# Kernel optimization log

Measured on AMD Instinct MI355X. Metric: run time of the kernel, lower is better.

## Reference

```python
import jax, jax.numpy as jnp
import numpy as np

S, B, D, H, DFF = 1024, 8, 1024, 16, 4096
HD = D // H
EPS = 1e-5


def layernorm(x, g, b):
    m = jnp.mean(x, axis=-1, keepdims=True)
    v = jnp.mean(jnp.square(x - m), axis=-1, keepdims=True)
    return (x - m) * jax.lax.rsqrt(v + EPS) * g + b


def setup_inputs() -> dict:
    key = jax.random.key(0)
    ks = jax.random.split(key, 6)
    w = 0.02
    return {
        "src": jax.random.normal(ks[0], (S, B, D), dtype=jnp.float32),
        "in_proj_w": jax.random.normal(ks[1], (3 * D, D), dtype=jnp.float32) * w,
        "in_proj_b": jnp.zeros((3 * D,), dtype=jnp.float32),
        "out_w": jax.random.normal(ks[2], (D, D), dtype=jnp.float32) * w,
        "out_b": jnp.zeros((D,), dtype=jnp.float32),
        "lin1_w": jax.random.normal(ks[3], (DFF, D), dtype=jnp.float32) * w,
        "lin1_b": jnp.zeros((DFF,), dtype=jnp.float32),
        "lin2_w": jax.random.normal(ks[4], (D, DFF), dtype=jnp.float32) * w,
        "lin2_b": jnp.zeros((D,), dtype=jnp.float32),
        "n1_g": jnp.ones((D,), dtype=jnp.float32),
        "n1_b": jnp.zeros((D,), dtype=jnp.float32),
        "n2_g": jnp.ones((D,), dtype=jnp.float32),
        "n2_b": jnp.zeros((D,), dtype=jnp.float32),
    }


def reference(src, in_proj_w, in_proj_b, out_w, out_b,
              lin1_w, lin1_b, lin2_w, lin2_b,
              n1_g, n1_b, n2_g, n2_b):
    # self-attention block (eval mode: dropout = identity)
    qkv = jnp.einsum('sbd,ed->sbe', src, in_proj_w) + in_proj_b  # [S,B,3D]
    q, k, v = jnp.split(qkv, 3, axis=-1)
    q = q.reshape(S, B, H, HD) * (1.0 / np.sqrt(HD)).astype(np.float32)
    k = k.reshape(S, B, H, HD)
    v = v.reshape(S, B, H, HD)
    scores = jnp.einsum('sbhd,tbhd->bhst', q, k)        # [B,H,S,S]
    attn = jax.nn.softmax(scores, axis=-1)
    o = jnp.einsum('bhst,tbhd->sbhd', attn, v).reshape(S, B, D)
    o = jnp.einsum('sbd,ed->sbe', o, out_w) + out_b
    # post-LN residuals
    x = layernorm(src + o, n1_g, n1_b)
    h = jax.nn.relu(jnp.einsum('sbd,fd->sbf', x, lin1_w) + lin1_b)
    f = jnp.einsum('sbf,df->sbd', h, lin2_w) + lin2_b
    return layernorm(x + f, n2_g, n2_b)
```

## Files before the change

### kernel.cpp

```cpp
#include <hip/hip_runtime.h>
#include <cstdint>
#include <cstddef>

#define S_  1024
#define B_  8
#define D_  1024
#define H_  16
#define HD_ 64
#define DFF_ 4096
#define M_  (S_*B_)
#define QKV_N (3*D_)

typedef float f32x4 __attribute__((ext_vector_type(4)));
typedef __bf16 bf16x8 __attribute__((ext_vector_type(8)));
typedef __bf16 bf16x4 __attribute__((ext_vector_type(4)));

#define GLDS16(gp, lp) __builtin_amdgcn_global_load_lds( \
    (__attribute__((address_space(1))) void*)(gp), \
    (__attribute__((address_space(3))) void*)(lp), 16, 0, 0)

#define CB0 (M_*D_/4)
#define CB1 (CB0 + QKV_N*D_/4)
#define CB2 (CB1 + D_*D_/4)
#define CB3 (CB2 + DFF_*D_/4)
#define CB4 (CB3 + D_*DFF_/4)

__global__ __launch_bounds__(256)
void cvt_all(const float* __restrict__ src, const float* __restrict__ w1f,
             const float* __restrict__ w2f, const float* __restrict__ w3f,
             const float* __restrict__ w4f,
             __bf16* __restrict__ src_bf, __bf16* __restrict__ w1,
             __bf16* __restrict__ w2, __bf16* __restrict__ w3,
             __bf16* __restrict__ w4)
{
    int i = blockIdx.x * 256 + threadIdx.x;
    const float* in; __bf16* out; int off;
    if      (i < CB0) { in = src; out = src_bf; off = 0;   }
    else if (i < CB1) { in = w1f; out = w1;     off = CB0; }
    else if (i < CB2) { in = w2f; out = w2;     off = CB1; }
    else if (i < CB3) { in = w3f; out = w3;     off = CB2; }
    else if (i < CB4) { in = w4f; out = w4;     off = CB3; }
    else return;
    int j = i - off;
    float4 v = *(const float4*)(in + (size_t)j * 4);
    __bf16 t[4] = {(__bf16)v.x, (__bf16)v.y, (__bf16)v.z, (__bf16)v.w};
    *(uint2*)(out + (size_t)j * 4) = *(uint2*)t;
}

template<bool OUT_BF16, bool RELU, bool ADD_BIAS, bool SPLITZ>
__global__ __launch_bounds__(512, 2)
void gemm8p(const __bf16* __restrict__ A, const __bf16* __restrict__ W,
            const float* __restrict__ bias,
            void* __restrict__ Cv0, void* __restrict__ Cv1,
            int N, int Kloop, int lda)
{
    extern __shared__ __bf16 lds[];

    const int tid  = threadIdx.x;
    const int lane = tid & 63;
    const int wv   = tid >> 6;
    const int quad = lane >> 4;
    const int l15  = lane & 15;
    const int wm   = (wv >> 2) * 128;
    const int wn   = (wv & 3) * 64;

    const int id  = blockIdx.y * gridDim.x + blockIdx.x;
    const int nwg = gridDim.x * gridDim.y;
    const int q8  = nwg >> 3;
    const int k   = (id & 7) * q8 + (id >> 3);
    const int within = k & 31;
    const int chunk  = k >> 5;
    const int nchm   = gridDim.x >> 3;
    const int cm     = chunk % nchm;
    const int cn     = chunk / nchm;
    const int m0 = (cm * 8 + (within & 7)) * 256;
    const int n0 = (cn * 4 + (within >> 3)) * 256;

    void* Cv = Cv0;
    if (SPLITZ) {
        const int koff = blockIdx.z * Kloop;
        A += koff;
        W += koff;
        if (blockIdx.z) Cv = Cv1;
    }

    const int nt = Kloop >> 6;

    const int crow = tid >> 2;
    const int csl  = (tid & 3) ^ ((crow >> 1) & 3);
    const __bf16* gA[2] = { A + (size_t)(m0 + crow) * lda + csl * 8,
                            A + (size_t)(m0 + 128 + crow) * lda + csl * 8 };
    const __bf16* gW[2] = { W + (size_t)(n0 + crow) * lda + csl * 8,
                            W + (size_t)(n0 + 128 + crow) * lda + csl * 8 };
    char* ldsSt = (char*)lds + tid * 16;

    #define CHA(kv, hh, kt) GLDS16(gA[hh] + ((kt) << 6) + (kv) * 32, \
        ldsSt + (((kt) & 1) * 65536 + (kv) * 16384 + (hh) * 8192))
    #define CHB(kv, hh, kt) GLDS16(gW[hh] + ((kt) << 6) + (kv) * 32, \
        ldsSt + (((kt) & 1) * 65536 + 32768 + (kv) * 16384 + (hh) * 8192))

    const int swzE = (quad ^ ((l15 >> 1) & 3)) * 8;
    const __bf16* aBase = lds + (wm + l15) * 32 + swzE;
    const __bf16* bBase = lds + 16384 + (wn + l15) * 32 + swzE;

    CHB(0,0,0); CHB(0,1,0); CHA(0,0,0); CHA(0,1,0);
    CHB(1,0,0); CHB(1,1,0); CHA(1,0,0); CHA(1,1,0);
    CHB(0,0,1); CHB(0,1,1); CHA(0,0,1); CHA(0,1,1);
    CHB(1,0,1); CHB(1,1,1);
    asm volatile("s_waitcnt vmcnt(6)" ::: "memory");
    __builtin_amdgcn_s_barrier();

    f32x4 acc[8][4] = {};

    #define KTILE(T, S1, S2, VM1, VM2) do { \
        const __bf16* aB = aBase + ((T) & 1) * 32768; \
        const __bf16* bB = bBase + ((T) & 1) * 32768; \
        bf16x8 b_[4], a_[4]; \
         \
        _Pragma("unroll") for (int j = 0; j < 4; ++j) b_[j] = *(const bf16x8*)(bB + j * 512); \
        _Pragma("unroll") for (int i = 0; i < 4; ++i) a_[i] = *(const bf16x8*)(aB + i * 512); \
        if (S1) { CHA(1,0,(T)+1); CHA(1,1,(T)+1); } \
        __builtin_amdgcn_s_barrier(); \
        asm volatile("s_waitcnt lgkmcnt(0)" ::: "memory"); \
        __builtin_amdgcn_s_setprio(1); \
        _Pragma("unroll") for (int i = 0; i < 4; ++i) \
            _Pragma("unroll") for (int j = 0; j < 4; ++j) \
                acc[i][j] = __builtin_amdgcn_mfma_f32_16x16x32_bf16(a_[i], b_[j], acc[i][j], 0, 0, 0); \
        __builtin_amdgcn_s_setprio(0); \
        __builtin_amdgcn_s_barrier(); \
         \
        _Pragma("unroll") for (int i = 0; i < 4; ++i) a_[i] = *(const bf16x8*)(aB + (i + 4) * 512); \
        if (S2) { CHB(0,0,(T)+2); CHB(0,1,(T)+2); } \
        __builtin_amdgcn_s_barrier(); \
        asm volatile("s_waitcnt lgkmcnt(0)" ::: "memory"); \
        __builtin_amdgcn_s_setprio(1); \
        _Pragma("unroll") for (int i = 0; i < 4; ++i) \
            _Pragma("unroll") for (int j = 0; j < 4; ++j) \
                acc[i+4][j] = __builtin_amdgcn_mfma_f32_16x16x32_bf16(a_[i], b_[j], acc[i+4][j], 0, 0, 0); \
        __builtin_amdgcn_s_setprio(0); \
        asm volatile("s_waitcnt vmcnt(" VM1 ")" ::: "memory"); \
        __builtin_amdgcn_s_barrier(); \
         \
        _Pragma("unroll") for (int j = 0; j < 4; ++j) b_[j] = *(const bf16x8*)(bB + 8192 + j * 512); \
        _Pragma("unroll") for (int i = 0; i < 4; ++i) a_[i] = *(const bf16x8*)(aB + 8192 + i * 512); \
        if (S2) { CHA(0,0,(T)+2); CHA(0,1,(T)+2); } \
        __builtin_amdgcn_s_barrier(); \
        asm volatile("s_waitcnt lgkmcnt(0)" ::: "memory"); \
        __builtin_amdgcn_s_setprio(1); \
        _Pragma("unroll") for (int i = 0; i < 4; ++i) \
            _Pragma("unroll") for (int j = 0; j < 4; ++j) \
                acc[i][j] = __builtin_amdgcn_mfma_f32_16x16x32_bf16(a_[i], b_[j], acc[i][j], 0, 0, 0); \
        __builtin_amdgcn_s_setprio(0); \
        __builtin_amdgcn_s_barrier(); \
         \
        _Pragma("unroll") for (int i = 0; i < 4; ++i) a_[i] = *(const bf16x8*)(aB + 8192 + (i + 4) * 512); \
        if (S2) { CHB(1,0,(T)+2); CHB(1,1,(T)+2); } \
        __builtin_amdgcn_s_barrier(); \
        asm volatile("s_waitcnt lgkmcnt(0)" ::: "memory"); \
        __builtin_amdgcn_s_setprio(1); \
        _Pragma("unroll") for (int i = 0; i < 4; ++i) \
            _Pragma("unroll") for (int j = 0; j < 4; ++j) \
                acc[i+4][j] = __builtin_amdgcn_mfma_f32_16x16x32_bf16(a_[i], b_[j], acc[i+4][j], 0, 0, 0); \
        __builtin_amdgcn_s_setprio(0); \
        asm volatile("s_waitcnt vmcnt(" VM2 ")" ::: "memory"); \
        __builtin_amdgcn_s_barrier(); \
    } while (0)

    for (int t = 0; t < nt - 2; ++t) KTILE(t, true, true, "10", "10");
    KTILE(nt - 2, true,  false, "8", "4");
    KTILE(nt - 1, false, false, "0", "0");

    #undef KTILE
    #undef CHA
    #undef CHB

    float bvj[4];
    #pragma unroll
    for (int j = 0; j < 4; ++j)
        bvj[j] = ADD_BIAS ? bias[n0 + wn + j * 16 + l15] : 0.f;
    const size_t cbase = (size_t)(m0 + wm + quad * 4) * N + (n0 + wn + l15);
    #pragma unroll
    for (int i = 0; i < 8; ++i) {
        #pragma unroll
        for (int r = 0; r < 4; ++r) {
            const size_t rowb = cbase + (size_t)(i * 16 + r) * N;
            #pragma unroll
            for (int j = 0; j < 4; ++j) {
                float v = acc[i][j][r] + bvj[j];
                if (RELU) v = fmaxf(v, 0.f);
                if (OUT_BF16)
                    ((__bf16*)Cv)[rowb + j * 16] = (__bf16)v;
                else
                    ((float*)Cv)[rowb + j * 16] = v;
            }
        }
    }
}

template<bool OUT_BF16, bool RELU, bool ADD_BIAS, bool SPLITZ>
__global__ __launch_bounds__(512, 4)
void gemm128(const __bf16* __restrict__ A, const __bf16* __restrict__ W,
             const float* __restrict__ bias,
             void* __restrict__ Cv0, void* __restrict__ Cv1,
             int N, int Kloop, int lda)
{
    extern __shared__ __bf16 lds[];

    const int tid  = threadIdx.x;
    const int lane = tid & 63;
    const int wv   = tid >> 6;
    const int quad = lane >> 4;
    const int l15  = lane & 15;
    const int wm   = (wv & 1) * 64;
    const int wn   = (wv >> 1) * 64;

    const int id  = blockIdx.y * gridDim.x + blockIdx.x;
    const int nwg = gridDim.x * gridDim.y;
    const int q8  = nwg >> 3;
    const int k   = (id & 7) * q8 + (id >> 3);
    const int within = k & 31;
    const int chunk  = k >> 5;
    const int nchm   = gridDim.x >> 3;
    const int cm     = chunk % nchm;
    const int cn     = chunk / nchm;
    const int m0 = (cm * 8 + (within & 7)) * 128;
    const int n0 = (cn * 4 + (within >> 3)) * 256;

    void* Cv = Cv0;
    if (SPLITZ) {
        const int koff = blockIdx.z * Kloop;
        A += koff;
        W += koff;
        if (blockIdx.z) Cv = Cv1;
    }

    const int nt = Kloop >> 5;

    const int crow = tid >> 2;
    const int csl  = (tid & 3) ^ ((crow >> 1) & 3);
    const __bf16* gA0 = A + (size_t)(m0 + crow) * lda + csl * 8;
    const __bf16* gW0 = W + (size_t)(n0 + crow) * lda + csl * 8;
    const __bf16* gW1 = gW0 + (size_t)128 * lda;
    char* ldsSt = (char*)lds + tid * 16;

    #define STAGE(kt, buf) do { \
        const int ko = (kt) << 5; \
        char* d_ = ldsSt + (buf) * 24576; \
        GLDS16(gW0 + ko, d_ + 8192); \
        GLDS16(gW1 + ko, d_ + 16384); \
        GLDS16(gA0 + ko, d_); \
    } while (0)

    const int swz = (quad ^ ((l15 >> 1) & 3)) * 8;
    const __bf16* aBase = lds + (wm + l15) * 32 + swz;
    const __bf16* bBase = lds + 4096 + (wn + l15) * 32 + swz;

    #define BARRIER_DRAIN() do { \
        asm volatile("s_waitcnt vmcnt(0)" ::: "memory"); \
        __builtin_amdgcn_s_barrier(); \
        __builtin_amdgcn_sched_barrier(0); \
    } while (0)

    STAGE(0, 0);
    BARRIER_DRAIN();

    f32x4 acc[4][4] = {};

    for (int t = 0; t < nt; ++t) {
        const int cur = t & 1;
        if (t + 1 < nt) STAGE(t + 1, cur ^ 1);

        const __bf16* aB = aBase + cur * 12288;
        const __bf16* bB = bBase + cur * 12288;
        bf16x8 b_[4];
        #pragma unroll
        for (int j = 0; j < 4; ++j)
            b_[j] = *(const bf16x8*)(bB + j * 512);
        __builtin_amdgcn_s_setprio(1);
        #pragma unroll
        for (int i = 0; i < 4; ++i) {
            bf16x8 a_ = *(const bf16x8*)(aB + i * 512);
            #pragma unroll
            for (int j = 0; j < 4; ++j)
                acc[i][j] = __builtin_amdgcn_mfma_f32_16x16x32_bf16(a_, b_[j], acc[i][j], 0, 0, 0);
        }
        __builtin_amdgcn_s_setprio(0);

        if (t + 1 < nt) BARRIER_DRAIN();
    }

    #undef BARRIER_DRAIN
    #undef STAGE

    float bvj[4];
    #pragma unroll
    for (int j = 0; j < 4; ++j)
        bvj[j] = ADD_BIAS ? bias[n0 + wn + j * 16 + l15] : 0.f;
    const size_t cbase = (size_t)(m0 + wm + quad * 4) * N + (n0 + wn + l15);
    #pragma unroll
    for (int i = 0; i < 4; ++i) {
        #pragma unroll
        for (int r = 0; r < 4; ++r) {
            const size_t rowb = cbase + (size_t)(i * 16 + r) * N;
            #pragma unroll
            for (int j = 0; j < 4; ++j) {
                float v = acc[i][j][r] + bvj[j];
                if (RELU) v = fmaxf(v, 0.f);
                if (OUT_BF16)
                    ((__bf16*)Cv)[rowb + j * 16] = (__bf16)v;
                else
                    ((float*)Cv)[rowb + j * 16] = v;
            }
        }
    }
}

__global__ __launch_bounds__(256)
void v_transpose(const __bf16* __restrict__ qkv, __bf16* __restrict__ vt)
{
    __shared__ __bf16 T[64 * 65];
    const int tid = threadIdx.x;
    const int t0  = blockIdx.x * 64;
    const int bh  = blockIdx.y;
    const int b   = bh & (B_ - 1);
    const int h   = bh / B_;

    #pragma unroll
    for (int j = 0; j < 2; ++j) {
        int c = j * 256 + tid;
        int i = c >> 3, cc = c & 7;
        const __bf16* g = qkv + (size_t)((t0 + i) * B_ + b) * QKV_N + 2 * D_ + h * HD_ + cc * 8;
        bf16x8 v = *(const bf16x8*)g;
        #pragma unroll
        for (int u = 0; u < 8; ++u) T[(cc * 8 + u) * 65 + i] = v[u];
    }
    __syncthreads();
    #pragma unroll
    for (int j = 0; j < 2; ++j) {
        int c = j * 256 + tid;
        int d = c >> 3, cc = c & 7;
        __bf16 pk[8];
        #pragma unroll
        for (int u = 0; u < 8; ++u) pk[u] = T[d * 65 + cc * 8 + u];
        *(uint4*)(vt + ((size_t)bh * HD_ + d) * S_ + t0 + cc * 8) = *(uint4*)pk;
    }
}

__global__ __launch_bounds__(512, 4)
void attn_flash(const __bf16* __restrict__ qkv, const __bf16* __restrict__ vt,
                __bf16* __restrict__ out)
{
    extern __shared__ __bf16 alds[];
    __bf16* Ks0 = alds;
    __bf16* Vs0 = alds + 16384;
    __bf16* Ps  = alds + 32768;

    const int tid  = threadIdx.x;
    const int lane = tid & 63;
    const int wv   = tid >> 6;
    const int quad = lane >> 4;
    const int l15  = lane & 15;

    const int id = blockIdx.y * gridDim.x + blockIdx.x;
    const int k  = (id & 7) * ((S_ / 128) * B_ * H_ / 8) + (id >> 3);
    const int s0 = (k & 7) * 128;
    const int bh = k >> 3;
    const int b  = bh & (B_ - 1);
    const int h  = bh / B_;

    const int i0k = tid >> 3, cck = tid & 7, scck = cck ^ (i0k & 7);
    const int i0v = tid >> 4, ccv = tid & 15, sccv = ccv ^ (i0v & 15);
    const __bf16* gK0 = qkv + ((size_t)i0k * B_ + b) * QKV_N + D_ + h * HD_ + scck * 8;
    const __bf16* gK1 = gK0 + (size_t)64 * B_ * QKV_N;
    const __bf16* gV0 = vt + ((size_t)bh * HD_ + i0v) * S_ + sccv * 8;
    const __bf16* gV1 = gV0 + (size_t)32 * S_;
    char* dK = (char*)Ks0 + tid * 16;
    char* dV = (char*)Vs0 + tid * 16;
    const size_t KADV = (size_t)128 * B_ * QKV_N;

    #define STAGEKV(buf) do { \
        GLDS16(gK0, dK + (buf) * 16384); \
        GLDS16(gK1, dK + (buf) * 16384 + 8192); \
        GLDS16(gV0, dV + (buf) * 16384); \
        GLDS16(gV1, dV + (buf) * 16384 + 8192); \
        gK0 += KADV; gK1 += KADV; gV0 += 128; gV1 += 128; \
    } while (0)

    STAGEKV(0);

    const int qrow = wv * 16 + l15;
    bf16x8 bq[2];
    #pragma unroll
    for (int kk = 0; kk < 2; ++kk)
        bq[kk] = *(const bf16x8*)(qkv + (size_t)((s0 + qrow) * B_ + b) * QKV_N
                                  + h * HD_ + kk * 32 + quad * 8);

    __syncthreads();

    f32x4 oacc[4] = {};
    float l_run = 0.f;
    const float C2 = 0.125f * 1.44269504f;
    const int xk = l15 & 7;
    const __bf16* psB = Ps + qrow * 64;

    const int nt2 = S_ / 128;
    for (int it = 0; it < nt2; ++it) {
        const int cur = it & 1;
        if (it + 1 < nt2) STAGEKV(cur ^ 1);

        #pragma unroll
        for (int s = 0; s < 2; ++s) {
            f32x4 sacc[4] = {};
            #pragma unroll
            for (int kk = 0; kk < 2; ++kk) {
                const __bf16* akB = Ks0 + cur * 8192 + s * 4096 + l15 * 64
                                    + (((kk * 4 + quad) ^ xk) * 8);
                #pragma unroll
                for (int j = 0; j < 4; ++j)
                    sacc[j] = __builtin_amdgcn_mfma_f32_16x16x32_bf16(
                        *(const bf16x8*)(akB + j * 1024), bq[kk], sacc[j], 0, 0, 0);
            }

            float rs = 0.f;
            #pragma unroll
            for (int j = 0; j < 4; ++j)
                #pragma unroll
                for (int r = 0; r < 4; ++r) {
                    float p = __builtin_amdgcn_exp2f(sacc[j][r] * C2);
                    sacc[j][r] = p;
                    rs += p;
                }
            rs += __shfl_xor(rs, 16, 64);
            rs += __shfl_xor(rs, 32, 64);
            l_run += rs;

            #pragma unroll
            for (int j = 0; j < 4; ++j) {
                __bf16 pk[4] = {(__bf16)sacc[j][0], (__bf16)sacc[j][1],
                                (__bf16)sacc[j][2], (__bf16)sacc[j][3]};
                int s16 = (j * 2 + (quad >> 1)) ^ xk;
                *(uint2*)(psB + s16 * 8 + (quad & 1) * 4) = *(uint2*)pk;
            }

            #pragma unroll
            for (int kk = 0; kk < 2; ++kk) {
                bf16x8 ap = *(const bf16x8*)(psB + (((kk * 4 + quad) ^ xk) * 8));
                const __bf16* bvB = Vs0 + cur * 8192 + l15 * 128
                                    + (((s * 8 + kk * 4 + quad) ^ l15) * 8);
                #pragma unroll
                for (int jd = 0; jd < 4; ++jd)
                    oacc[jd] = __builtin_amdgcn_mfma_f32_16x16x32_bf16(
                        ap, *(const bf16x8*)(bvB + jd * 2048), oacc[jd], 0, 0, 0);
            }
        }

        __syncthreads();
    }
    #undef STAGEKV

    float linv = 1.f / l_run;
    #pragma unroll
    for (int r = 0; r < 4; ++r) {
        float lr = __shfl(linv, quad * 4 + r, 64);
        int s = s0 + wv * 16 + quad * 4 + r;
        #pragma unroll
        for (int jd = 0; jd < 4; ++jd) {
            int d = jd * 16 + l15;
            out[(size_t)(s * B_ + b) * D_ + h * HD_ + d] = (__bf16)(oacc[jd][r] * lr);
        }
    }
}

__global__ __launch_bounds__(256)
void ln_res3(const float* __restrict__ xa, const __bf16* __restrict__ p0,
             const __bf16* __restrict__ p1, const float* __restrict__ bias,
             const float* __restrict__ g, const float* __restrict__ beta,
             float* __restrict__ yout, __bf16* __restrict__ ybf)
{
    __shared__ float red[8];
    const int row = blockIdx.x;
    const int tid = threadIdx.x;
    const size_t base = (size_t)row * D_ + tid * 4;

    float4 a  = *(const float4*)(xa + base);
    bf16x4 q0 = *(const bf16x4*)(p0 + base);
    bf16x4 q1 = *(const bf16x4*)(p1 + base);
    float4 bb = *(const float4*)(bias + tid * 4);
    float x0 = a.x + (float)q0[0] + (float)q1[0] + bb.x;
    float x1 = a.y + (float)q0[1] + (float)q1[1] + bb.y;
    float x2 = a.z + (float)q0[2] + (float)q1[2] + bb.z;
    float x3 = a.w + (float)q0[3] + (float)q1[3] + bb.w;

    float s  = x0 + x1 + x2 + x3;
    float ss = x0 * x0 + x1 * x1 + x2 * x2 + x3 * x3;
    for (int msk = 1; msk <= 32; msk <<= 1) {
        s  += __shfl_xor(s,  msk, 64);
        ss += __shfl_xor(ss, msk, 64);
    }
    const int wv = tid >> 6;
    if ((tid & 63) == 0) { red[wv] = s; red[4 + wv] = ss; }
    __syncthreads();
    s  = red[0] + red[1] + red[2] + red[3];
    ss = red[4] + red[5] + red[6] + red[7];
    float mean = s * (1.f / D_);
    float var  = ss * (1.f / D_) - mean * mean;
    float rstd = rsqrtf(var + 1e-5f);

    float4 gv = *(const float4*)(g + tid * 4);
    float4 bv = *(const float4*)(beta + tid * 4);
    float y0 = (x0 - mean) * rstd * gv.x + bv.x;
    float y1 = (x1 - mean) * rstd * gv.y + bv.y;
    float y2 = (x2 - mean) * rstd * gv.z + bv.z;
    float y3 = (x3 - mean) * rstd * gv.w + bv.w;
    *(float4*)(yout + base) = make_float4(y0, y1, y2, y3);
    if (ybf) {
        __bf16 t[4] = {(__bf16)y0, (__bf16)y1, (__bf16)y2, (__bf16)y3};
        *(uint2*)(ybf + base) = *(uint2*)t;
    }
}

extern "C" void kernel_launch(void* const* d_in, const int* in_sizes, int n_in,
                              void* d_out, int out_size, void* d_ws, size_t ws_size,
                              hipStream_t stream)
{
    const float* src       = (const float*)d_in[0];
    const float* in_proj_w = (const float*)d_in[1];
    const float* in_proj_b = (const float*)d_in[2];
    const float* out_w     = (const float*)d_in[3];
    const float* out_b     = (const float*)d_in[4];
    const float* lin1_w    = (const float*)d_in[5];
    const float* lin1_b    = (const float*)d_in[6];
    const float* lin2_w    = (const float*)d_in[7];
    const float* lin2_b    = (const float*)d_in[8];
    const float* n1_g = (const float*)d_in[9];
    const float* n1_b = (const float*)d_in[10];
    const float* n2_g = (const float*)d_in[11];
    const float* n2_b = (const float*)d_in[12];

    char* ws = (char*)d_ws;
    size_t off = 0;
    auto alloc = [&](size_t bytes) { char* p = ws + off; off += (bytes + 255) & ~(size_t)255; return p; };

    __bf16* src_bf = (__bf16*)alloc((size_t)M_ * D_ * 2);
    __bf16* w1     = (__bf16*)alloc((size_t)QKV_N * D_ * 2);
    __bf16* w2     = (__bf16*)alloc((size_t)D_ * D_ * 2);
    __bf16* w3     = (__bf16*)alloc((size_t)DFF_ * D_ * 2);
    __bf16* w4     = (__bf16*)alloc((size_t)D_ * DFF_ * 2);
    __bf16* qkv    = (__bf16*)alloc((size_t)M_ * QKV_N * 2);
    char*   h_r    = alloc((size_t)M_ * DFF_ * 2);
    __bf16* xbf    = (__bf16*)alloc((size_t)M_ * D_ * 2);
    float*  xf     = (float*)alloc((size_t)M_ * D_ * 4);
    __bf16* vt     = (__bf16*)alloc((size_t)B_ * H_ * HD_ * S_ * 2);

    const size_t PART = (size_t)M_ * D_;
    __bf16* attn_o = src_bf;
    __bf16* o0 = (__bf16*)h_r;
    __bf16* o1 = o0 + PART;
    __bf16* hbf = (__bf16*)h_r;
    __bf16* f0 = vt;
    __bf16* f1 = xbf;

    const size_t SHM8  = 131072;
    const size_t SHM2  = 49152;
    const size_t ASHM  = 81920;

    cvt_all<<<(CB4 + 255) / 256, 256, 0, stream>>>(
        src, in_proj_w, out_w, lin1_w, lin2_w, src_bf, w1, w2, w3, w4);

    gemm128<true, false, true, false><<<dim3(M_ / 128, QKV_N / 256), 512, SHM2, stream>>>(
        src_bf, w1, in_proj_b, qkv, nullptr, QKV_N, D_, D_);

    v_transpose<<<dim3(S_ / 64, B_ * H_), 256, 0, stream>>>(qkv, vt);

    attn_flash<<<dim3(S_ / 128, B_ * H_), 512, ASHM, stream>>>(qkv, vt, attn_o);

    gemm8p<true, false, false, true><<<dim3(M_ / 256, D_ / 256, 2), 512, SHM8, stream>>>(
        attn_o, w2, nullptr, o0, o1, D_, D_ / 2, D_);

    ln_res3<<<M_, 256, 0, stream>>>(src, o0, o1, out_b, n1_g, n1_b, xf, xbf);

    gemm8p<true, true, true, false><<<dim3(M_ / 256, DFF_ / 256), 512, SHM8, stream>>>(
        xbf, w3, lin1_b, hbf, nullptr, DFF_, D_, D_);

    gemm8p<true, false, false, true><<<dim3(M_ / 256, D_ / 256, 2), 512, SHM8, stream>>>(
        hbf, w4, nullptr, f0, f1, D_, DFF_ / 2, DFF_);

    ln_res3<<<M_, 256, 0, stream>>>(xf, f0, f1, lin2_b, n2_g, n2_b, (float*)d_out, nullptr);
}
```

Measured before the change: 451.0 us.

## Add triple-buffered 256x256 GEMM kernel for attention output projection

Introduces a new gemm256 kernel that stages K-slices of 32 into a three-slot LDS ring (96KB) with direct global-to-LDS loads. It prefetches two tiles ahead and double-buffers A fragments in registers so MFMA work overlaps loads, with raised wave priority around the MFMA bursts. It replaces gemm8p only for the split-K out-projection GEMM. The smaller LDS footprint may allow two blocks per CU, but the larger register arrays may limit occupancy.

Measured after the change: 443.9 us. No clear change (-1.6%).

```diff
diff --git a/kernel.cpp b/kernel.cpp
--- a/kernel.cpp
+++ b/kernel.cpp
@@ -198,6 +198,148 @@
 }
 
 template<bool OUT_BF16, bool RELU, bool ADD_BIAS, bool SPLITZ>
+__global__ __launch_bounds__(512, 2)
+void gemm256(const __bf16* __restrict__ A, const __bf16* __restrict__ W,
+             const float* __restrict__ bias,
+             void* __restrict__ Cv0, void* __restrict__ Cv1,
+             int N, int Kloop, int lda)
+{
+    extern __shared__ __bf16 lds[];
+
+    const int tid  = threadIdx.x;
+    const int lane = tid & 63;
+    const int wv   = tid >> 6;
+    const int quad = lane >> 4;
+    const int l15  = lane & 15;
+    const int wm   = (wv >> 2) * 128;
+    const int wn   = (wv & 3) * 64;
+
+    const int id  = blockIdx.y * gridDim.x + blockIdx.x;
+    const int nwg = gridDim.x * gridDim.y;
+    const int q8  = nwg >> 3;
+    const int k   = (id & 7) * q8 + (id >> 3);
+    const int within = k & 31;
+    const int chunk  = k >> 5;
+    const int nchm   = gridDim.x >> 3;
+    const int cm     = chunk % nchm;
+    const int cn     = chunk / nchm;
+    const int m0 = (cm * 8 + (within & 7)) * 256;
+    const int n0 = (cn * 4 + (within >> 3)) * 256;
+
+    void* Cv = Cv0;
+    if (SPLITZ) {
+        const int koff = blockIdx.z * Kloop;
+        A += koff;
+        W += koff;
+        if (blockIdx.z) Cv = Cv1;
+    }
+
+    const int nt = Kloop >> 5;
+
+    const int crow = tid >> 2;
+    const int csl  = (tid & 3) ^ ((crow >> 1) & 3);
+    const __bf16* gA0 = A + (size_t)(m0 + crow) * lda + csl * 8;
+    const __bf16* gA1 = gA0 + (size_t)128 * lda;
+    const __bf16* gW0 = W + (size_t)(n0 + crow) * lda + csl * 8;
+    const __bf16* gW1 = gW0 + (size_t)128 * lda;
+    char* ldsSt = (char*)lds + tid * 16;
+
+    #define STAGE(kt, buf) do { \
+        const int ko = (kt) << 5; \
+        char* d_ = ldsSt + (buf) * 32768; \
+        GLDS16(gW0 + ko, d_ + 16384); \
+        GLDS16(gW1 + ko, d_ + 24576); \
+        GLDS16(gA0 + ko, d_); \
+        GLDS16(gA1 + ko, d_ + 8192); \
+    } while (0)
+
+    const int swz = (quad ^ ((l15 >> 1) & 3)) * 8;
+    const __bf16* aBase = lds + (wm + l15) * 32 + swz;
+    const __bf16* bBase = lds + 8192 + (wn + l15) * 32 + swz;
+
+    #define RDA_ALL(arr, buf) do { const __bf16* p_ = aBase + (buf) * 16384; \
+        _Pragma("unroll") for (int i_ = 0; i_ < 8; ++i_) \
+            arr[i_] = *(const bf16x8*)(p_ + i_ * 512); } while (0)
+    #define RDB_ALL(arr, buf) do { const __bf16* p_ = bBase + (buf) * 16384; \
+        _Pragma("unroll") for (int j_ = 0; j_ < 4; ++j_) \
+            arr[j_] = *(const bf16x8*)(p_ + j_ * 512); } while (0)
+
+    #define BARRIER_DRAIN() do { \
+        asm volatile("s_waitcnt vmcnt(0)" ::: "memory"); \
+        __builtin_amdgcn_s_barrier(); \
+        __builtin_amdgcn_sched_barrier(0); \
+    } while (0)
+
+    STAGE(0, 0);
+    STAGE(1, 1);
+    BARRIER_DRAIN();
+
+    f32x4 acc[8][4] = {};
+    bf16x8 aP[8], aN[8], b_[4];
+
+    RDA_ALL(aP, 0);
+
+    int b_cur = 0;
+    for (int t = 0; t < nt; t += 2) {
+        int b_nxt = b_cur + 1; if (b_nxt == 3) b_nxt = 0;
+        int b_st  = b_nxt + 1; if (b_st  == 3) b_st  = 0;
+
+        if (t + 2 < nt) STAGE(t + 2, b_st);
+        RDB_ALL(b_, b_cur);
+        RDA_ALL(aN, b_nxt);
+        __builtin_amdgcn_s_setprio(1);
+        #pragma unroll
+        for (int i = 0; i < 8; ++i)
+            #pragma unroll
+            for (int j = 0; j < 4; ++j)
+                acc[i][j] = __builtin_amdgcn_mfma_f32_16x16x32_bf16(aP[i], b_[j], acc[i][j], 0, 0, 0);
+        __builtin_amdgcn_s_setprio(0);
+        BARRIER_DRAIN();
+
+        if (t + 3 < nt) STAGE(t + 3, b_cur);
+        RDB_ALL(b_, b_nxt);
+        if (t + 2 < nt) RDA_ALL(aP, b_st);
+        __builtin_amdgcn_s_setprio(1);
+        #pragma unroll
+        for (int i = 0; i < 8; ++i)
+            #pragma unroll
+            for (int j = 0; j < 4; ++j)
+                acc[i][j] = __builtin_amdgcn_mfma_f32_16x16x32_bf16(aN[i], b_[j], acc[i][j], 0, 0, 0);
+        __builtin_amdgcn_s_setprio(0);
+        if (t + 2 < nt) BARRIER_DRAIN();
+
+        b_cur = b_st;
+    }
+
+    #undef BARRIER_DRAIN
+    #undef RDA_ALL
+    #undef RDB_ALL
+    #undef STAGE
+
+    float bvj[4];
+    #pragma unroll
+    for (int j = 0; j < 4; ++j)
+        bvj[j] = ADD_BIAS ? bias[n0 + wn + j * 16 + l15] : 0.f;
+    const size_t cbase = (size_t)(m0 + wm + quad * 4) * N + (n0 + wn + l15);
+    #pragma unroll
+    for (int i = 0; i < 8; ++i) {
+        #pragma unroll
+        for (int r = 0; r < 4; ++r) {
+            const size_t rowb = cbase + (size_t)(i * 16 + r) * N;
+            #pragma unroll
+            for (int j = 0; j < 4; ++j) {
+                float v = acc[i][j][r] + bvj[j];
+                if (RELU) v = fmaxf(v, 0.f);
+                if (OUT_BF16)
+                    ((__bf16*)Cv)[rowb + j * 16] = (__bf16)v;
+                else
+                    ((float*)Cv)[rowb + j * 16] = v;
+            }
+        }
+    }
+}
+
+template<bool OUT_BF16, bool RELU, bool ADD_BIAS, bool SPLITZ>
 __global__ __launch_bounds__(512, 4)
 void gemm128(const __bf16* __restrict__ A, const __bf16* __restrict__ W,
              const float* __restrict__ bias,
@@ -561,6 +703,7 @@
     __bf16* f1 = xbf;
 
     const size_t SHM8  = 131072;
+    const size_t SHM3  = 98304;
     const size_t SHM2  = 49152;
     const size_t ASHM  = 81920;
 
@@ -574,7 +717,7 @@
 
     attn_flash<<<dim3(S_ / 128, B_ * H_), 512, ASHM, stream>>>(qkv, vt, attn_o);
 
-    gemm8p<true, false, false, true><<<dim3(M_ / 256, D_ / 256, 2), 512, SHM8, stream>>>(
+    gemm256<true, false, false, true><<<dim3(M_ / 256, D_ / 256, 2), 512, SHM3, stream>>>(
         attn_o, w2, nullptr, o0, o1, D_, D_ / 2, D_);
 
     ln_res3<<<M_, 256, 0, stream>>>(src, o0, o1, out_b, n1_g, n1_b, xf, xbf);
```
